# Kernel optimization log

Measured on AMD Instinct MI355X. Metric: run time of the kernel, lower is better.

Reference implementation:

```python
import jax, jax.numpy as jnp
import numpy as np

N_EMBD = 512
BLOCK_SIZE = 512
NUM_HEADS = 8
HEAD_SIZE = 64
ROPE_BASE = 10000.0


def apply_rope(x):
    # x: [B, H, T, D]; rotates interleaved pairs with position = token index.
    B, H, T, D = x.shape
    half = D // 2
    inv_freq = 1.0 / (ROPE_BASE ** (jnp.arange(half, dtype=jnp.float32) * 2.0 / D))
    ang = jnp.arange(T, dtype=jnp.float32)[:, None] * inv_freq[None, :]  # [T, half]
    cos = jnp.cos(ang).astype(x.dtype)  # [T, half]
    sin = jnp.sin(ang).astype(x.dtype)
    x1 = x[..., 0::2]  # [B,H,T,half]
    x2 = x[..., 1::2]
    o1 = x1 * cos - x2 * sin
    o2 = x2 * cos + x1 * sin
    return jnp.stack([o1, o2], axis=-1).reshape(B, H, T, D)


def setup_inputs() -> dict:
    key = jax.random.key(0)
    ks = jax.random.split(key, 6)
    B, T, C = 32, 512, N_EMBD
    HD = NUM_HEADS * HEAD_SIZE
    s_in = 1.0 / np.sqrt(C)
    s_out = 1.0 / np.sqrt(HD)
    return {
        "x": jax.random.normal(ks[0], (B, T, C), dtype=jnp.float32),
        "Wq": jax.random.normal(ks[1], (C, HD), dtype=jnp.float32) * s_in,
        "Wk": jax.random.normal(ks[2], (C, HD), dtype=jnp.float32) * s_in,
        "Wv": jax.random.normal(ks[3], (C, HD), dtype=jnp.float32) * s_in,
        "Wo": jax.random.normal(ks[4], (HD, C), dtype=jnp.float32) * s_out,
        "bo": jax.random.normal(ks[5], (C,), dtype=jnp.float32) * 0.01,
    }


def reference(x, Wq, Wk, Wv, Wo, bo):
    B, T, C = x.shape
    H, D = NUM_HEADS, HEAD_SIZE
    # projections -> [B, H, T, D]
    q = (x @ Wq).reshape(B, T, H, D).transpose(0, 2, 1, 3)
    k = (x @ Wk).reshape(B, T, H, D).transpose(0, 2, 1, 3)
    v = (x @ Wv).reshape(B, T, H, D).transpose(0, 2, 1, 3)
    q = apply_rope(q)
    k = apply_rope(k)
    scale = 1.0 / np.sqrt(D)
    wei = jnp.einsum('bhqd,bhkd->bhqk', q, k) * scale  # [B,H,T,T]
    causal = jnp.tril(jnp.ones((T, T), dtype=bool))
    wei = jnp.where(causal, wei, -jnp.inf)
    wei = jax.nn.softmax(wei, axis=-1)
    # dropout omitted (eval mode / deterministic baseline)
    out = jnp.einsum('bhqk,bhkd->bhqd', wei, v)  # [B,H,T,D]
    out = out.transpose(0, 2, 1, 3).reshape(B, T, H * D)
    return out @ Wo + bo
```

## Files before the change

kernel.cpp:

```cpp
#include <hip/hip_runtime.h>

#define TSEQ 512
#define CDIM 512
#define NH 8
#define HS 64
#define BBATCH 32
#define MROWS (BBATCH * TSEQ)

typedef unsigned short u16;
typedef __bf16 bf16x8 __attribute__((ext_vector_type(8)));
typedef float f32x4 __attribute__((ext_vector_type(4)));
typedef float f32x16 __attribute__((ext_vector_type(16)));

__device__ __forceinline__ u16 f2b(float f) {
  union { float f; unsigned u; } v; v.f = f;
  unsigned r = (v.u + 0x7fffu + ((v.u >> 16) & 1u)) >> 16;
  return (u16)r;
}

__device__ __forceinline__ void gload_lds16(const u16* g, u16* l) {
  __builtin_amdgcn_global_load_lds(
      (const __attribute__((address_space(1))) void*)g,
      (__attribute__((address_space(3))) void*)l, 16, 0, 0);
}


__global__ __launch_bounds__(256) void conv_x(const float* __restrict__ x,
                                              u16* __restrict__ A2) {
  __shared__ __align__(16) u16 tile[128][136];
  const int tid = threadIdx.x;
  const int m0 = blockIdx.x * 128;
  const int cc = blockIdx.y;
#pragma unroll
  for (int i = 0; i < 16; ++i) {
    int idx = i * 256 + tid;
    int ml = idx >> 5, c4 = idx & 31;
    float4 v = *reinterpret_cast<const float4*>(
        x + (size_t)(m0 + ml) * CDIM + cc * 128 + c4 * 4);
    ushort4 o; o.x = f2b(v.x); o.y = f2b(v.y); o.z = f2b(v.z); o.w = f2b(v.w);
    *reinterpret_cast<ushort4*>(&tile[ml][c4 * 4]) = o;
  }
  __syncthreads();
#pragma unroll
  for (int i = 0; i < 8; ++i) {
    int uid = i * 256 + tid;
    int kb = uid >> 7, ml = uid & 127;
    int4 v = *reinterpret_cast<const int4*>(&tile[ml][kb * 8]);
    *reinterpret_cast<int4*>(A2 + ((size_t)(cc * 16 + kb) * MROWS + m0 + ml) * 8) = v;
  }
}

__global__ __launch_bounds__(256) void transpose_w(const float* __restrict__ wq,
                                                   const float* __restrict__ wk,
                                                   const float* __restrict__ wv,
                                                   const float* __restrict__ wo,
                                                   u16* __restrict__ B2,
                                                   u16* __restrict__ B2o) {
  __shared__ __align__(16) u16 tile[64][136];
  const int tid = threadIdx.x;
  int mat = blockIdx.z;
  const float* src = (mat == 0) ? wq : (mat == 1) ? wk : (mat == 2) ? wv : wo;
  u16* dst = (mat < 3) ? (B2 + (size_t)mat * 64 * 512 * 8) : B2o;
  const int k0 = blockIdx.x * 64, n0 = blockIdx.y * 128;
#pragma unroll
  for (int i = 0; i < 8; ++i) {
    int idx = i * 256 + tid;
    int kl = idx >> 5, c4 = idx & 31;
    float4 v = *reinterpret_cast<const float4*>(
        src + (size_t)(k0 + kl) * CDIM + n0 + c4 * 4);
    ushort4 o; o.x = f2b(v.x); o.y = f2b(v.y); o.z = f2b(v.z); o.w = f2b(v.w);
    *reinterpret_cast<ushort4*>(&tile[kl][c4 * 4]) = o;
  }
  __syncthreads();
#pragma unroll
  for (int i = 0; i < 4; ++i) {
    int uid = i * 256 + tid;
    int kb = uid >> 7, nl = uid & 127;
    ushort4 lo, hi;
    lo.x = tile[kb * 8 + 0][nl]; lo.y = tile[kb * 8 + 1][nl];
    lo.z = tile[kb * 8 + 2][nl]; lo.w = tile[kb * 8 + 3][nl];
    hi.x = tile[kb * 8 + 4][nl]; hi.y = tile[kb * 8 + 5][nl];
    hi.z = tile[kb * 8 + 6][nl]; hi.w = tile[kb * 8 + 7][nl];
    u16* d = dst + ((size_t)(k0 / 8 + kb) * 512 + n0 + nl) * 8;
    *reinterpret_cast<ushort4*>(d) = lo;
    *reinterpret_cast<ushort4*>(d + 4) = hi;
  }
}

__global__ __launch_bounds__(256) void rope_tab(float* __restrict__ cosT,
                                                float* __restrict__ sinT) {
  int i = blockIdx.x * 256 + threadIdx.x;
  int t = i >> 5, f = i & 31;
  float inv = __powf(10000.0f, -(float)f / 32.0f);
  float ang = (float)t * inv;
  cosT[i] = cosf(ang);
  sinT[i] = sinf(ang);
}

__global__ __launch_bounds__(256) void vt_t(const u16* __restrict__ Vb,
                                            u16* __restrict__ VT) {
  __shared__ __align__(16) u16 tile[64][72];
  const int bh = blockIdx.x;
  const int b = bh >> 3, h = bh & 7;
  const int tt = blockIdx.y;
  const int tid = threadIdx.x;
#pragma unroll
  for (int p = 0; p < 2; ++p) {
    int tl = (tid >> 3) + p * 32;
    int dc = tid & 7;
    const u16* src = Vb + (size_t)(b * TSEQ + tt * 64 + tl) * CDIM + h * HS + dc * 8;
    ushort4 v0 = *reinterpret_cast<const ushort4*>(src);
    ushort4 v1 = *reinterpret_cast<const ushort4*>(src + 4);
    tile[dc * 8 + 0][tl] = v0.x; tile[dc * 8 + 1][tl] = v0.y;
    tile[dc * 8 + 2][tl] = v0.z; tile[dc * 8 + 3][tl] = v0.w;
    tile[dc * 8 + 4][tl] = v1.x; tile[dc * 8 + 5][tl] = v1.y;
    tile[dc * 8 + 6][tl] = v1.z; tile[dc * 8 + 7][tl] = v1.w;
  }
  __syncthreads();
#pragma unroll
  for (int p = 0; p < 2; ++p) {
    int d = (tid >> 3) + p * 32;
    int tc = tid & 7;
    int4 vdat = *reinterpret_cast<const int4*>(&tile[d][tc * 8]);
    *reinterpret_cast<int4*>(VT + (size_t)(bh * HS + d) * TSEQ + tt * 64 + tc * 8) = vdat;
  }
}

__global__ __launch_bounds__(256, 2) void qkv_gemm(const u16* __restrict__ A2,
                                                   const u16* __restrict__ B2,
                                                   const float* __restrict__ cosT,
                                                   const float* __restrict__ sinT,
                                                   u16* __restrict__ Qb,
                                                   u16* __restrict__ Kb,
                                                   u16* __restrict__ Vb) {
  __shared__ __align__(16) u16 lds[2][16384];
  const int tid = threadIdx.x;
  const int lane = tid & 63;
  const int l31 = lane & 31, hh = lane >> 5;
  const int wid = tid >> 6;
  const int wmb = (wid >> 1) * 64, wnb = (wid & 1) * 64;
  const int m0 = blockIdx.x * 128;
  const int n0 = blockIdx.y * 128;
  const int mat = n0 >> 9;
  const int nc0 = n0 & 511;
  const u16* B2m = B2 + (size_t)mat * (64 * 512 * 8);

  f32x16 acc[2][2] = {};

  auto stage = [&](int buf, int t) {
#pragma unroll
    for (int c = 0; c < 4; ++c) {
      int u = c * 256 + tid;
      int kb = u >> 7, ml = u & 127;
      gload_lds16(A2 + ((size_t)(t * 8 + kb) * MROWS + m0 + ml) * 8,
                  &lds[buf][u * 8]);
    }
#pragma unroll
    for (int c = 0; c < 4; ++c) {
      int u = c * 256 + tid;
      int kb = u >> 7, nl = u & 127;
      gload_lds16(B2m + ((size_t)(t * 8 + kb) * 512 + nc0 + nl) * 8,
                  &lds[buf][8192 + u * 8]);
    }
  };

  stage(0, 0);
  asm volatile("s_waitcnt vmcnt(0)" ::: "memory");
  __builtin_amdgcn_sched_barrier(0);
  __builtin_amdgcn_s_barrier();
  __builtin_amdgcn_sched_barrier(0);
  int cur = 0;
  for (int t = 0; t < 8; ++t) {
    if (t + 1 < 8) stage(cur ^ 1, t + 1);
    const u16* LA = &lds[cur][0];
    const u16* LB = &lds[cur][8192];
#pragma unroll
    for (int ks = 0; ks < 4; ++ks) {
      int kb2 = ks * 2 + hh;
      bf16x8 a0 = *reinterpret_cast<const bf16x8*>(LA + (kb2 * 128 + wmb + l31) * 8);
      bf16x8 a1 = *reinterpret_cast<const bf16x8*>(LA + (kb2 * 128 + wmb + 32 + l31) * 8);
      bf16x8 b0 = *reinterpret_cast<const bf16x8*>(LB + (kb2 * 128 + wnb + l31) * 8);
      bf16x8 b1 = *reinterpret_cast<const bf16x8*>(LB + (kb2 * 128 + wnb + 32 + l31) * 8);
      acc[0][0] = __builtin_amdgcn_mfma_f32_32x32x16_bf16(a0, b0, acc[0][0], 0, 0, 0);
      acc[0][1] = __builtin_amdgcn_mfma_f32_32x32x16_bf16(a0, b1, acc[0][1], 0, 0, 0);
      acc[1][0] = __builtin_amdgcn_mfma_f32_32x32x16_bf16(a1, b0, acc[1][0], 0, 0, 0);
      acc[1][1] = __builtin_amdgcn_mfma_f32_32x32x16_bf16(a1, b1, acc[1][1], 0, 0, 0);
    }
    __builtin_amdgcn_sched_barrier(0);
    asm volatile("s_waitcnt vmcnt(0)" ::: "memory");
    __builtin_amdgcn_s_barrier();
    __builtin_amdgcn_sched_barrier(0);
    cur ^= 1;
  }

  if (mat < 2) {
    u16* dst = (mat == 0) ? Qb : Kb;
#pragma unroll
    for (int nr = 0; nr < 2; ++nr) {
      int nc = nc0 + wnb + nr * 32 + l31;
      int fi = (nc & 63) >> 1;
      int odd = nc & 1;
#pragma unroll
      for (int mr = 0; mr < 2; ++mr)
#pragma unroll
        for (int r = 0; r < 16; ++r) {
          int row = m0 + wmb + mr * 32 + (r & 3) + 8 * (r >> 2) + 4 * hh;
          int tq = row & (TSEQ - 1);
          float v = acc[mr][nr][r];
          float o = __shfl_xor(v, 1);
          float c = cosT[tq * 32 + fi], sn = sinT[tq * 32 + fi];
          float res = odd ? (v * c + o * sn) : (v * c - o * sn);
          dst[(size_t)row * CDIM + nc] = f2b(res);
        }
    }
  } else {
#pragma unroll
    for (int nr = 0; nr < 2; ++nr) {
      int nc = nc0 + wnb + nr * 32 + l31;
#pragma unroll
      for (int mr = 0; mr < 2; ++mr)
#pragma unroll
        for (int r = 0; r < 16; ++r) {
          int row = m0 + wmb + mr * 32 + (r & 3) + 8 * (r >> 2) + 4 * hh;
          Vb[(size_t)row * CDIM + nc] = f2b(acc[mr][nr][r]);
        }
    }
  }
}

__global__ __launch_bounds__(128, 4) void attn_kern(const u16* __restrict__ Qb,
                                                    const u16* __restrict__ Kb,
                                                    const u16* __restrict__ VT,
                                                    u16* __restrict__ A2out) {
  const int lane = threadIdx.x & 63, wid = threadIdx.x >> 6;
  const int l31 = lane & 31, hh = lane >> 5;
  const int bh = blockIdx.x, b = bh >> 3, h = bh & 7;
  const int q0 = blockIdx.y * 64 + wid * 32;

  bf16x8 qf[4];
  const u16* qbase = Qb + (size_t)(b * TSEQ + q0 + l31) * CDIM + h * HS + hh * 8;
#pragma unroll
  for (int ds = 0; ds < 4; ++ds)
    qf[ds] = *reinterpret_cast<const bf16x8*>(qbase + ds * 16);

  const float SC = 0.125f * 1.4426950408889634f;
  float m_r = -1e30f, lsum = 0.0f;
  f32x16 of[2] = {};

  const int nkt = (q0 >> 5) + 1;
  for (int kt = 0; kt < nkt; ++kt) {
    f32x16 s = {};
    const u16* kr = Kb + (size_t)(b * TSEQ + kt * 32 + l31) * CDIM + h * HS + hh * 8;
#pragma unroll
    for (int ds = 0; ds < 4; ++ds) {
      bf16x8 kf = *reinterpret_cast<const bf16x8*>(kr + ds * 16);
      s = __builtin_amdgcn_mfma_f32_32x32x16_bf16(kf, qf[ds], s, 0, 0, 0);
    }
    float p[16];
#pragma unroll
    for (int r = 0; r < 16; ++r) p[r] = s[r] * SC;
    if (kt == nkt - 1) {
#pragma unroll
      for (int r = 0; r < 16; ++r) {
        int kk = (r & 3) + 8 * (r >> 2) + 4 * hh;
        if (kk > l31) p[r] = -1e30f;
      }
    }
    float pm = p[0];
#pragma unroll
    for (int r = 1; r < 16; ++r) pm = fmaxf(pm, p[r]);
    pm = fmaxf(pm, __shfl_xor(pm, 32));
    if (!__all(pm - m_r <= 8.0f)) {
      float mn = fmaxf(m_r, pm);
      float alpha = exp2f(m_r - mn);
      m_r = mn;
      lsum *= alpha;
#pragma unroll
      for (int r = 0; r < 16; ++r) { of[0][r] *= alpha; of[1][r] *= alpha; }
    }
    float ts = 0.0f;
#pragma unroll
    for (int r = 0; r < 16; ++r) { p[r] = exp2f(p[r] - m_r); ts += p[r]; }
    ts += __shfl_xor(ts, 32);
    lsum += ts;

    unsigned w0, w1, w2, w3, w4, w5, w6, w7;
    asm("v_cvt_pk_bf16_f32 %0, %1, %2" : "=v"(w0) : "v"(p[0]),  "v"(p[1]));
    asm("v_cvt_pk_bf16_f32 %0, %1, %2" : "=v"(w1) : "v"(p[2]),  "v"(p[3]));
    asm("v_cvt_pk_bf16_f32 %0, %1, %2" : "=v"(w2) : "v"(p[4]),  "v"(p[5]));
    asm("v_cvt_pk_bf16_f32 %0, %1, %2" : "=v"(w3) : "v"(p[6]),  "v"(p[7]));
    asm("v_cvt_pk_bf16_f32 %0, %1, %2" : "=v"(w4) : "v"(p[8]),  "v"(p[9]));
    asm("v_cvt_pk_bf16_f32 %0, %1, %2" : "=v"(w5) : "v"(p[10]), "v"(p[11]));
    asm("v_cvt_pk_bf16_f32 %0, %1, %2" : "=v"(w6) : "v"(p[12]), "v"(p[13]));
    asm("v_cvt_pk_bf16_f32 %0, %1, %2" : "=v"(w7) : "v"(p[14]), "v"(p[15]));
    asm("v_permlane32_swap_b32 %0, %1" : "+v"(w0), "+v"(w2));
    asm("v_permlane32_swap_b32 %0, %1" : "+v"(w1), "+v"(w3));
    asm("v_permlane32_swap_b32 %0, %1" : "+v"(w4), "+v"(w6));
    asm("v_permlane32_swap_b32 %0, %1" : "+v"(w5), "+v"(w7));
    union { unsigned u[4]; bf16x8 v; } pb0, pb1;
    pb0.u[0] = w0; pb0.u[1] = w1; pb0.u[2] = w2; pb0.u[3] = w3;
    pb1.u[0] = w4; pb1.u[1] = w5; pb1.u[2] = w6; pb1.u[3] = w7;

    const u16* vr = VT + (size_t)(bh * HS + l31) * TSEQ + kt * 32 + hh * 8;
    bf16x8 vf00 = *reinterpret_cast<const bf16x8*>(vr);
    bf16x8 vf01 = *reinterpret_cast<const bf16x8*>(vr + 16);
    bf16x8 vf10 = *reinterpret_cast<const bf16x8*>(vr + 32 * TSEQ);
    bf16x8 vf11 = *reinterpret_cast<const bf16x8*>(vr + 32 * TSEQ + 16);
    of[0] = __builtin_amdgcn_mfma_f32_32x32x16_bf16(vf00, pb0.v, of[0], 0, 0, 0);
    of[0] = __builtin_amdgcn_mfma_f32_32x32x16_bf16(vf01, pb1.v, of[0], 0, 0, 0);
    of[1] = __builtin_amdgcn_mfma_f32_32x32x16_bf16(vf10, pb0.v, of[1], 0, 0, 0);
    of[1] = __builtin_amdgcn_mfma_f32_32x32x16_bf16(vf11, pb1.v, of[1], 0, 0, 0);
  }

  float inv = 1.0f / lsum;
  const int grow = b * TSEQ + q0 + l31;
#pragma unroll
  for (int dt = 0; dt < 2; ++dt)
#pragma unroll
    for (int i = 0; i < 8; ++i) {
      ushort2 st;
      st.x = f2b(of[dt][2 * i] * inv);
      st.y = f2b(of[dt][2 * i + 1] * inv);
      int kb = h * 8 + dt * 4 + ((2 * i) >> 2);
      int off = ((2 * i) & 3) + 4 * hh;
      *reinterpret_cast<ushort2*>(
          A2out + ((size_t)kb * MROWS + grow) * 8 + off) = st;
    }
}

__global__ __launch_bounds__(256, 2) void out_gemm(const u16* __restrict__ A2,
                                                   const u16* __restrict__ B2o,
                                                   const float* __restrict__ bias,
                                                   float* __restrict__ out) {
  __shared__ __align__(16) u16 lds[2][16384];
  const int tid = threadIdx.x;
  const int lane = tid & 63;
  const int l31 = lane & 31, hh = lane >> 5;
  const int wid = tid >> 6;
  const int wmb = (wid >> 1) * 64, wnb = (wid & 1) * 64;
  const int m0 = blockIdx.x * 128;
  const int n0 = blockIdx.y * 128;

  f32x16 acc[2][2] = {};

  auto stage = [&](int buf, int t) {
#pragma unroll
    for (int c = 0; c < 4; ++c) {
      int u = c * 256 + tid;
      int kb = u >> 7, ml = u & 127;
      gload_lds16(A2 + ((size_t)(t * 8 + kb) * MROWS + m0 + ml) * 8,
                  &lds[buf][u * 8]);
    }
#pragma unroll
    for (int c = 0; c < 4; ++c) {
      int u = c * 256 + tid;
      int kb = u >> 7, nl = u & 127;
      gload_lds16(B2o + ((size_t)(t * 8 + kb) * 512 + n0 + nl) * 8,
                  &lds[buf][8192 + u * 8]);
    }
  };

  stage(0, 0);
  asm volatile("s_waitcnt vmcnt(0)" ::: "memory");
  __builtin_amdgcn_sched_barrier(0);
  __builtin_amdgcn_s_barrier();
  __builtin_amdgcn_sched_barrier(0);
  int cur = 0;
  for (int t = 0; t < 8; ++t) {
    if (t + 1 < 8) stage(cur ^ 1, t + 1);
    const u16* LA = &lds[cur][0];
    const u16* LB = &lds[cur][8192];
#pragma unroll
    for (int ks = 0; ks < 4; ++ks) {
      int kb2 = ks * 2 + hh;
      bf16x8 a0 = *reinterpret_cast<const bf16x8*>(LA + (kb2 * 128 + wmb + l31) * 8);
      bf16x8 a1 = *reinterpret_cast<const bf16x8*>(LA + (kb2 * 128 + wmb + 32 + l31) * 8);
      bf16x8 b0 = *reinterpret_cast<const bf16x8*>(LB + (kb2 * 128 + wnb + l31) * 8);
      bf16x8 b1 = *reinterpret_cast<const bf16x8*>(LB + (kb2 * 128 + wnb + 32 + l31) * 8);
      acc[0][0] = __builtin_amdgcn_mfma_f32_32x32x16_bf16(a0, b0, acc[0][0], 0, 0, 0);
      acc[0][1] = __builtin_amdgcn_mfma_f32_32x32x16_bf16(a0, b1, acc[0][1], 0, 0, 0);
      acc[1][0] = __builtin_amdgcn_mfma_f32_32x32x16_bf16(a1, b0, acc[1][0], 0, 0, 0);
      acc[1][1] = __builtin_amdgcn_mfma_f32_32x32x16_bf16(a1, b1, acc[1][1], 0, 0, 0);
    }
    __builtin_amdgcn_sched_barrier(0);
    asm volatile("s_waitcnt vmcnt(0)" ::: "memory");
    __builtin_amdgcn_s_barrier();
    __builtin_amdgcn_sched_barrier(0);
    cur ^= 1;
  }

#pragma unroll
  for (int nr = 0; nr < 2; ++nr) {
    int col = n0 + wnb + nr * 32 + l31;
    float bv = bias[col];
#pragma unroll
    for (int mr = 0; mr < 2; ++mr)
#pragma unroll
      for (int r = 0; r < 16; ++r) {
        int row = m0 + wmb + mr * 32 + (r & 3) + 8 * (r >> 2) + 4 * hh;
        out[(size_t)row * CDIM + col] = acc[mr][nr][r] + bv;
      }
  }
}

extern "C" void kernel_launch(void* const* d_in, const int* in_sizes, int n_in,
                              void* d_out, int out_size, void* d_ws, size_t ws_size,
                              hipStream_t stream) {
  const float* x  = (const float*)d_in[0];
  const float* Wq = (const float*)d_in[1];
  const float* Wk = (const float*)d_in[2];
  const float* Wv = (const float*)d_in[3];
  const float* Wo = (const float*)d_in[4];
  const float* bo = (const float*)d_in[5];
  float* out = (float*)d_out;

  char* p = (char*)d_ws;
  const size_t big = (size_t)MROWS * CDIM * 2;
  u16* A2x  = (u16*)p; p += big;
  u16* B2   = (u16*)p; p += (size_t)3 * 64 * 512 * 8 * 2;
  u16* B2o  = (u16*)p; p += (size_t)64 * 512 * 8 * 2;
  float* cosT = (float*)p; p += (size_t)TSEQ * 32 * 4;
  float* sinT = (float*)p; p += (size_t)TSEQ * 32 * 4;
  u16* Qb   = (u16*)p; p += big;
  u16* Kb   = (u16*)p; p += big;
  u16* VT   = (u16*)p; p += big;
  u16* Vb   = (u16*)p; p += big;

  hipLaunchKernelGGL(conv_x, dim3(MROWS / 128, 4), dim3(256), 0, stream, x, A2x);
  hipLaunchKernelGGL(transpose_w, dim3(8, 4, 4), dim3(256), 0, stream,
                     Wq, Wk, Wv, Wo, B2, B2o);
  hipLaunchKernelGGL(rope_tab, dim3(TSEQ * 32 / 256), dim3(256), 0, stream, cosT, sinT);
  hipLaunchKernelGGL(qkv_gemm, dim3(MROWS / 128, 1536 / 128), dim3(256), 0, stream,
                     A2x, B2, cosT, sinT, Qb, Kb, Vb);
  hipLaunchKernelGGL(vt_t, dim3(BBATCH * NH, TSEQ / 64), dim3(256), 0, stream, Vb, VT);
  hipLaunchKernelGGL(attn_kern, dim3(BBATCH * NH, TSEQ / 64), dim3(128), 0, stream,
                     Qb, Kb, VT, A2x);
  hipLaunchKernelGGL(out_gemm, dim3(MROWS / 128, CDIM / 128), dim3(256), 0, stream,
                     A2x, B2o, bo, out);
}
```

Baseline: 111.8 us.

## Pre-pack K and V into MFMA fragment order for contiguous attention loads

Adds a kpack kernel and changes the V transpose kernel so K and V are written per 32-key tile in the exact per-lane MFMA operand order. Each lane in the attention loop then reads a contiguous 64-byte run instead of strided rows, which is meant to improve coalescing and cut memory transactions. The cost is an extra kernel launch and an extra pass over K. Kf reuses the Vb buffer, which is safe only because vt_t finishes reading Vb before kpack runs on the same stream.

```diff
diff --git a/kernel.cpp b/kernel.cpp
--- a/kernel.cpp
+++ b/kernel.cpp
@@ -98,7 +98,7 @@
 }
 
 __global__ __launch_bounds__(256) void vt_t(const u16* __restrict__ Vb,
-                                            u16* __restrict__ VT) {
+                                            u16* __restrict__ Vf) {
   __shared__ __align__(16) u16 tile[64][72];
   const int bh = blockIdx.x;
   const int b = bh >> 3, h = bh & 7;
@@ -117,12 +117,30 @@
     tile[dc * 8 + 6][tl] = v1.z; tile[dc * 8 + 7][tl] = v1.w;
   }
   __syncthreads();
+  const int lane = tid & 63, u = tid >> 6;
+  const int l31f = lane & 31, hhf = lane >> 5;
 #pragma unroll
   for (int p = 0; p < 2; ++p) {
-    int d = (tid >> 3) + p * 32;
-    int tc = tid & 7;
-    int4 vdat = *reinterpret_cast<const int4*>(&tile[d][tc * 8]);
-    *reinterpret_cast<int4*>(VT + (size_t)(bh * HS + d) * TSEQ + tt * 64 + tc * 8) = vdat;
+    int d = l31f + (u >> 1) * 32;
+    int toff = p * 32 + hhf * 8 + (u & 1) * 16;
+    int4 v = *reinterpret_cast<const int4*>(&tile[d][toff]);
+    *reinterpret_cast<int4*>(
+        Vf + (((size_t)bh * 16 + tt * 2 + p) * 64 + lane) * 32 + u * 8) = v;
+  }
+}
+
+__global__ __launch_bounds__(64) void kpack(const u16* __restrict__ Kb,
+                                            u16* __restrict__ Kf) {
+  const int lane = threadIdx.x;
+  const int l31 = lane & 31, hh = lane >> 5;
+  const int bh = blockIdx.x, b = bh >> 3, h = bh & 7;
+  const int kt = blockIdx.y;
+  const u16* kr = Kb + (size_t)(b * TSEQ + kt * 32 + l31) * CDIM + h * HS + hh * 8;
+  u16* dst = Kf + (((size_t)bh * 16 + kt) * 64 + lane) * 32;
+#pragma unroll
+  for (int ds = 0; ds < 4; ++ds) {
+    int4 v = *reinterpret_cast<const int4*>(kr + ds * 16);
+    *reinterpret_cast<int4*>(dst + ds * 8) = v;
   }
 }
 
@@ -229,8 +247,8 @@
 }
 
 __global__ __launch_bounds__(128, 4) void attn_kern(const u16* __restrict__ Qb,
-                                                    const u16* __restrict__ Kb,
-                                                    const u16* __restrict__ VT,
+                                                    const u16* __restrict__ Kf,
+                                                    const u16* __restrict__ Vf,
                                                     u16* __restrict__ A2out) {
   const int lane = threadIdx.x & 63, wid = threadIdx.x >> 6;
   const int l31 = lane & 31, hh = lane >> 5;
@@ -249,11 +267,11 @@
 
   const int nkt = (q0 >> 5) + 1;
   for (int kt = 0; kt < nkt; ++kt) {
+    const u16* kfr = Kf + (((size_t)bh * 16 + kt) * 64 + lane) * 32;
     f32x16 s = {};
-    const u16* kr = Kb + (size_t)(b * TSEQ + kt * 32 + l31) * CDIM + h * HS + hh * 8;
 #pragma unroll
     for (int ds = 0; ds < 4; ++ds) {
-      bf16x8 kf = *reinterpret_cast<const bf16x8*>(kr + ds * 16);
+      bf16x8 kf = *reinterpret_cast<const bf16x8*>(kfr + ds * 8);
       s = __builtin_amdgcn_mfma_f32_32x32x16_bf16(kf, qf[ds], s, 0, 0, 0);
     }
     float p[16];
@@ -301,11 +319,11 @@
     pb0.u[0] = w0; pb0.u[1] = w1; pb0.u[2] = w2; pb0.u[3] = w3;
     pb1.u[0] = w4; pb1.u[1] = w5; pb1.u[2] = w6; pb1.u[3] = w7;
 
-    const u16* vr = VT + (size_t)(bh * HS + l31) * TSEQ + kt * 32 + hh * 8;
-    bf16x8 vf00 = *reinterpret_cast<const bf16x8*>(vr);
-    bf16x8 vf01 = *reinterpret_cast<const bf16x8*>(vr + 16);
-    bf16x8 vf10 = *reinterpret_cast<const bf16x8*>(vr + 32 * TSEQ);
-    bf16x8 vf11 = *reinterpret_cast<const bf16x8*>(vr + 32 * TSEQ + 16);
+    const u16* vfr = Vf + (((size_t)bh * 16 + kt) * 64 + lane) * 32;
+    bf16x8 vf00 = *reinterpret_cast<const bf16x8*>(vfr);
+    bf16x8 vf01 = *reinterpret_cast<const bf16x8*>(vfr + 8);
+    bf16x8 vf10 = *reinterpret_cast<const bf16x8*>(vfr + 16);
+    bf16x8 vf11 = *reinterpret_cast<const bf16x8*>(vfr + 24);
     of[0] = __builtin_amdgcn_mfma_f32_32x32x16_bf16(vf00, pb0.v, of[0], 0, 0, 0);
     of[0] = __builtin_amdgcn_mfma_f32_32x32x16_bf16(vf01, pb1.v, of[0], 0, 0, 0);
     of[1] = __builtin_amdgcn_mfma_f32_32x32x16_bf16(vf10, pb0.v, of[1], 0, 0, 0);
@@ -423,8 +441,9 @@
   float* sinT = (float*)p; p += (size_t)TSEQ * 32 * 4;
   u16* Qb   = (u16*)p; p += big;
   u16* Kb   = (u16*)p; p += big;
-  u16* VT   = (u16*)p; p += big;
+  u16* Vf   = (u16*)p; p += big;
   u16* Vb   = (u16*)p; p += big;
+  u16* Kf   = Vb;
 
   hipLaunchKernelGGL(conv_x, dim3(MROWS / 128, 4), dim3(256), 0, stream, x, A2x);
   hipLaunchKernelGGL(transpose_w, dim3(8, 4, 4), dim3(256), 0, stream,
@@ -432,9 +451,10 @@
   hipLaunchKernelGGL(rope_tab, dim3(TSEQ * 32 / 256), dim3(256), 0, stream, cosT, sinT);
   hipLaunchKernelGGL(qkv_gemm, dim3(MROWS / 128, 1536 / 128), dim3(256), 0, stream,
                      A2x, B2, cosT, sinT, Qb, Kb, Vb);
-  hipLaunchKernelGGL(vt_t, dim3(BBATCH * NH, TSEQ / 64), dim3(256), 0, stream, Vb, VT);
+  hipLaunchKernelGGL(vt_t, dim3(BBATCH * NH, TSEQ / 64), dim3(256), 0, stream, Vb, Vf);
+  hipLaunchKernelGGL(kpack, dim3(BBATCH * NH, 16), dim3(64), 0, stream, Kb, Kf);
   hipLaunchKernelGGL(attn_kern, dim3(BBATCH * NH, TSEQ / 64), dim3(128), 0, stream,
-                     Qb, Kb, VT, A2x);
+                     Qb, Kf, Vf, A2x);
   hipLaunchKernelGGL(out_gemm, dim3(MROWS / 128, CDIM / 128), dim3(256), 0, stream,
                      A2x, B2o, bo, out);
 }
```

Result: slower. 115.4 us (+3.2%).
